# Kernel optimization log

Hardware: AMD Instinct MI355X
Metric: run time of the kernel (lower is better)

Reference implementation:

```python
import jax, jax.numpy as jnp
import numpy as np

F_CNT, V_CNT = 1024, 512
H, W = 192, 192
FX, FY = 200.0, 200.0
CX, CY = W / 2.0, H / 2.0
EPS = 1e-8


def quat_to_rot(q):
    # WXYZ quaternion -> rotation matrix, with normalization.
    q = q / (jnp.linalg.norm(q, axis=-1, keepdims=True) + EPS)
    w, x, y, z = q[..., 0], q[..., 1], q[..., 2], q[..., 3]
    return jnp.stack([
        jnp.stack([1 - 2 * (y * y + z * z), 2 * (x * y - w * z), 2 * (x * z + w * y)], -1),
        jnp.stack([2 * (x * y + w * z), 1 - 2 * (x * x + z * z), 2 * (y * z - w * x)], -1),
        jnp.stack([2 * (x * z - w * y), 2 * (y * z + w * x), 1 - 2 * (x * x + y * y)], -1),
    ], -2)


def rot_to_quat(R):
    # Branchless rotation matrix -> WXYZ quaternion.
    m00, m11, m22 = R[..., 0, 0], R[..., 1, 1], R[..., 2, 2]
    qw = 0.5 * jnp.sqrt(jnp.maximum(EPS, 1 + m00 + m11 + m22))
    qx = 0.5 * jnp.sqrt(jnp.maximum(EPS, 1 + m00 - m11 - m22))
    qy = 0.5 * jnp.sqrt(jnp.maximum(EPS, 1 - m00 + m11 - m22))
    qz = 0.5 * jnp.sqrt(jnp.maximum(EPS, 1 - m00 - m11 + m22))
    qx = jnp.copysign(qx, R[..., 2, 1] - R[..., 1, 2])
    qy = jnp.copysign(qy, R[..., 0, 2] - R[..., 2, 0])
    qz = jnp.copysign(qz, R[..., 1, 0] - R[..., 0, 1])
    return jnp.stack([qw, qx, qy, qz], -1)


def get_face_coord(a, b, c):
    # Per-face orthonormal frame (columns = x,y,z axes) and centroid.
    t = (a + b + c) / 3.0
    e1, e2 = b - a, c - a
    x = e1 / (jnp.linalg.norm(e1, axis=-1, keepdims=True) + EPS)
    n = jnp.cross(e1, e2)
    z = n / (jnp.linalg.norm(n, axis=-1, keepdims=True) + EPS)
    y = jnp.cross(z, x)
    return jnp.stack([x, y, z], -1), t


def render_gaussians(means, rot_qs, scales, colors, opac):
    # Differentiable 3DGS-style render: project, build 2D conics, depth-sorted
    # alpha compositing over all gaussians per pixel, white background.
    Rn = quat_to_rot(rot_qs)                      # [F,3,3]
    M = Rn * scales[:, None, :]                   # R @ diag(s)
    cov3 = M @ jnp.swapaxes(M, -1, -2)            # [F,3,3]
    X, Y, Z = means[:, 0], means[:, 1], means[:, 2]
    valid = (Z > 0.2).astype(means.dtype)
    Zc = jnp.maximum(Z, 0.2)
    mx = FX * X / Zc + CX
    my = FY * Y / Zc + CY
    zero = jnp.zeros_like(Zc)
    J = jnp.stack([
        jnp.stack([FX / Zc, zero, -FX * X / (Zc * Zc)], -1),
        jnp.stack([zero, FY / Zc, -FY * Y / (Zc * Zc)], -1),
    ], -2)                                        # [F,2,3]
    cov2 = J @ cov3 @ jnp.swapaxes(J, -1, -2)     # [F,2,2]
    a = cov2[:, 0, 0] + 0.3                       # low-pass dilation (3DGS)
    b = cov2[:, 0, 1]
    c = cov2[:, 1, 1] + 0.3
    det = jnp.maximum(a * c - b * b, EPS)
    conA, conB, conC = c / det, -b / det, a / det
    ys, xs = jnp.meshgrid(jnp.arange(H, dtype=means.dtype),
                          jnp.arange(W, dtype=means.dtype), indexing='ij')
    px, py = xs.reshape(-1), ys.reshape(-1)       # [HW]
    dx = px[None, :] - mx[:, None]                # [F,HW]
    dy = py[None, :] - my[:, None]
    power = -0.5 * (conA[:, None] * dx * dx + conC[:, None] * dy * dy) - conB[:, None] * dx * dy
    alpha = jnp.clip(opac[:, None] * jnp.exp(jnp.minimum(power, 0.0)), 0.0, 0.99) * valid[:, None]
    order = jnp.argsort(Zc)                       # front-to-back
    alpha = alpha[order]
    cols = colors[order]
    T = jnp.cumprod(1.0 - alpha, axis=0)
    T_excl = jnp.concatenate([jnp.ones_like(T[:1]), T[:-1]], axis=0)
    w = alpha * T_excl                            # [F,HW]
    img = jnp.einsum('fp,fc->cp', w, cols) + (1.0 - jnp.sum(w, 0))[None, :]
    return img.reshape(colors.shape[1], H, W)


def setup_inputs() -> dict:
    ks = jax.random.split(jax.random.key(0), 8)
    vp = jax.random.normal(ks[0], (V_CNT, 3), jnp.float32) * 0.5
    vp = vp.at[:, 2].add(5.0)  # put the mesh in front of the camera
    return {
        'img': jax.random.uniform(ks[1], (3, H, W), jnp.float32),
        'mask': jax.random.uniform(ks[2], (H, W), jnp.float32),
        'vertex_positions': vp,
        'faces': jax.random.randint(ks[3], (F_CNT, 3), 0, V_CNT, jnp.int32),
        'gp_rot_qs': jax.random.normal(ks[4], (F_CNT, 4), jnp.float32),
        'gp_log_scales': jax.random.normal(ks[5], (F_CNT, 3), jnp.float32) * 0.1 - 3.0,
        'gp_colors': jax.random.uniform(ks[6], (F_CNT, 3), jnp.float32),
        'gp_log_opacities': jnp.zeros((F_CNT, 1), jnp.float32),
    }


def reference(img, mask, vertex_positions, faces, gp_rot_qs, gp_log_scales,
              gp_colors, gp_log_opacities):
    vps_a = vertex_positions[faces[:, 0]]
    vps_b = vertex_positions[faces[:, 1]]
    vps_c = vertex_positions[faces[:, 2]]
    face_rs, face_ts = get_face_coord(vps_a, vps_b, vps_c)      # [F,3,3],[F,3]
    gp_scales = jnp.exp(gp_log_scales)
    gp_rot_mats = quat_to_rot(gp_rot_qs)
    # rows = scaled columns of the rotation (exactly as the torch code stacks)
    gp_rs = jnp.stack([gp_rot_mats[:, :, 0] * gp_scales[:, 0:1],
                       gp_rot_mats[:, :, 1] * gp_scales[:, 1:2],
                       gp_rot_mats[:, :, 2] * gp_scales[:, 2:3]], -2)
    global_gp_rs = face_rs @ gp_rs                               # merge_rt, gp_t = 0
    global_gp_ts = face_ts
    global_scales = jnp.linalg.norm(global_gp_rs, axis=-2)      # column norms [F,3]
    global_rot = global_gp_rs / (global_scales[:, None, :] + EPS)
    global_qs = rot_to_quat(global_rot)
    opac = jnp.exp(gp_log_opacities)[:, 0]
    rendered = render_gaussians(global_gp_ts, global_qs, global_scales, gp_colors, opac)
    mask_ = mask[None]
    masked_img = (1.0 - mask_) + img * mask_                     # white bg composite
    rgb_loss = jnp.mean((rendered - masked_img) ** 2)
    return rendered, rgb_loss
```

## Files before the change

kernel.cpp:

```cpp
#include <hip/hip_runtime.h>
#include <hip/hip_fp16.h>
#include <math.h>

#define F_CNT 1024
#define H_IMG 192
#define W_IMG 192
#define HW (H_IMG * W_IMG)
#define EPSF 1e-8f
#define N_SEG 8
#define SEG_LEN 128
#define HALF_PX 72
#define PIX_PER_BLK 144
#define LOG2E 1.4426950408889634f

#define RCP(x) __builtin_amdgcn_rcpf(x)


__device__ __forceinline__ unsigned long long prep_face(
    const int f,
    const float* __restrict__ vp,
    const int*   __restrict__ faces,
    const float* __restrict__ rot_qs,
    const float* __restrict__ log_scales,
    const float* __restrict__ colors,
    const float* __restrict__ log_opac,
    float sp[8][F_CNT])
{
    const int ia = faces[3 * f + 0], ib = faces[3 * f + 1], ic = faces[3 * f + 2];
    const float Ax = vp[3 * ia + 0], Ay = vp[3 * ia + 1], Az = vp[3 * ia + 2];
    const float Bx = vp[3 * ib + 0], By = vp[3 * ib + 1], Bz = vp[3 * ib + 2];
    const float Cx = vp[3 * ic + 0], Cy = vp[3 * ic + 1], Cz = vp[3 * ic + 2];

    const float tx = (Ax + Bx + Cx) / 3.0f;
    const float ty = (Ay + By + Cy) / 3.0f;
    const float tz = (Az + Bz + Cz) / 3.0f;

    const float e1x = Bx - Ax, e1y = By - Ay, e1z = Bz - Az;
    const float e2x = Cx - Ax, e2y = Cy - Ay, e2z = Cz - Az;

    const float rn1 = RCP(sqrtf(e1x * e1x + e1y * e1y + e1z * e1z) + EPSF);
    const float ux = e1x * rn1, uy = e1y * rn1, uz = e1z * rn1;
    const float cnx = e1y * e2z - e1z * e2y;
    const float cny = e1z * e2x - e1x * e2z;
    const float cnz = e1x * e2y - e1y * e2x;
    const float rn2 = RCP(sqrtf(cnx * cnx + cny * cny + cnz * cnz) + EPSF);
    const float wxv = cnx * rn2, wyv = cny * rn2, wzv = cnz * rn2;
    const float vx = wyv * uz - wzv * uy;
    const float vy = wzv * ux - wxv * uz;
    const float vz = wxv * uy - wyv * ux;

    const float q0 = rot_qs[4 * f + 0], q1 = rot_qs[4 * f + 1];
    const float q2 = rot_qs[4 * f + 2], q3 = rot_qs[4 * f + 3];
    const float rqn = RCP(sqrtf(q0 * q0 + q1 * q1 + q2 * q2 + q3 * q3) + EPSF);
    const float qw = q0 * rqn, qx = q1 * rqn, qy = q2 * rqn, qz = q3 * rqn;
    const float R00 = 1.0f - 2.0f * (qy * qy + qz * qz);
    const float R01 = 2.0f * (qx * qy - qw * qz);
    const float R02 = 2.0f * (qx * qz + qw * qy);
    const float R10 = 2.0f * (qx * qy + qw * qz);
    const float R11 = 1.0f - 2.0f * (qx * qx + qz * qz);
    const float R12 = 2.0f * (qy * qz - qw * qx);
    const float R20 = 2.0f * (qx * qz - qw * qy);
    const float R21 = 2.0f * (qy * qz + qw * qx);
    const float R22 = 1.0f - 2.0f * (qx * qx + qy * qy);

    const float s0 = expf(log_scales[3 * f + 0]);
    const float s1 = expf(log_scales[3 * f + 1]);
    const float s2 = expf(log_scales[3 * f + 2]);

    float G00, G10, G20, G01, G11, G21, G02, G12, G22;
    {
        float c0 = s0 * R00, c1 = s1 * R01, c2 = s2 * R02;
        G00 = ux * c0 + vx * c1 + wxv * c2;
        G10 = uy * c0 + vy * c1 + wyv * c2;
        G20 = uz * c0 + vz * c1 + wzv * c2;
    }
    {
        float c0 = s0 * R10, c1 = s1 * R11, c2 = s2 * R12;
        G01 = ux * c0 + vx * c1 + wxv * c2;
        G11 = uy * c0 + vy * c1 + wyv * c2;
        G21 = uz * c0 + vz * c1 + wzv * c2;
    }
    {
        float c0 = s0 * R20, c1 = s1 * R21, c2 = s2 * R22;
        G02 = ux * c0 + vx * c1 + wxv * c2;
        G12 = uy * c0 + vy * c1 + wyv * c2;
        G22 = uz * c0 + vz * c1 + wzv * c2;
    }

    const float gs0 = sqrtf(G00 * G00 + G10 * G10 + G20 * G20);
    const float gs1 = sqrtf(G01 * G01 + G11 * G11 + G21 * G21);
    const float gs2 = sqrtf(G02 * G02 + G12 * G12 + G22 * G22);
    const float rd0 = RCP(gs0 + EPSF), rd1 = RCP(gs1 + EPSF), rd2 = RCP(gs2 + EPSF);
    const float r00 = G00 * rd0, r10 = G10 * rd0, r20 = G20 * rd0;
    const float r01 = G01 * rd1, r11 = G11 * rd1, r21 = G21 * rd1;
    const float r02 = G02 * rd2, r12 = G12 * rd2, r22 = G22 * rd2;

    const float Qw = 0.5f * sqrtf(fmaxf(EPSF, 1.0f + r00 + r11 + r22));
    const float Qx = copysignf(0.5f * sqrtf(fmaxf(EPSF, 1.0f + r00 - r11 - r22)), r21 - r12);
    const float Qy = copysignf(0.5f * sqrtf(fmaxf(EPSF, 1.0f - r00 + r11 - r22)), r02 - r20);
    const float Qz = copysignf(0.5f * sqrtf(fmaxf(EPSF, 1.0f - r00 - r11 + r22)), r10 - r01);

    const float rqn2 = RCP(sqrtf(Qw * Qw + Qx * Qx + Qy * Qy + Qz * Qz) + EPSF);
    const float pw = Qw * rqn2, px = Qx * rqn2, py = Qy * rqn2, pz = Qz * rqn2;
    const float N00 = 1.0f - 2.0f * (py * py + pz * pz);
    const float N01 = 2.0f * (px * py - pw * pz);
    const float N02 = 2.0f * (px * pz + pw * py);
    const float N10 = 2.0f * (px * py + pw * pz);
    const float N11 = 1.0f - 2.0f * (px * px + pz * pz);
    const float N12 = 2.0f * (py * pz - pw * px);
    const float N20 = 2.0f * (px * pz - pw * py);
    const float N21 = 2.0f * (py * pz + pw * px);
    const float N22 = 1.0f - 2.0f * (px * px + py * py);

    const float M00 = N00 * gs0, M01 = N01 * gs1, M02 = N02 * gs2;
    const float M10 = N10 * gs0, M11 = N11 * gs1, M12 = N12 * gs2;
    const float M20 = N20 * gs0, M21 = N21 * gs1, M22 = N22 * gs2;
    const float C00 = M00 * M00 + M01 * M01 + M02 * M02;
    const float C01 = M00 * M10 + M01 * M11 + M02 * M12;
    const float C02 = M00 * M20 + M01 * M21 + M02 * M22;
    const float C11 = M10 * M10 + M11 * M11 + M12 * M12;
    const float C12 = M10 * M20 + M11 * M21 + M12 * M22;
    const float C22 = M20 * M20 + M21 * M21 + M22 * M22;

    const float valid = (tz > 0.2f) ? 1.0f : 0.0f;
    const float Zc = fmaxf(tz, 0.2f);
    const float rZc = RCP(Zc);
    const float mx = 200.0f * tx * rZc + 96.0f;
    const float my = 200.0f * ty * rZc + 96.0f;
    const float j00 = 200.0f * rZc;
    const float j02 = -200.0f * tx * (rZc * rZc);
    const float j11 = 200.0f * rZc;
    const float j12 = -200.0f * ty * (rZc * rZc);
    const float v00 = j00 * j00 * C00 + 2.0f * j00 * j02 * C02 + j02 * j02 * C22 + 0.3f;
    const float v01 = j00 * j11 * C01 + j00 * j12 * C02 + j02 * j11 * C12 + j02 * j12 * C22;
    const float v11 = j11 * j11 * C11 + 2.0f * j11 * j12 * C12 + j12 * j12 * C22 + 0.3f;
    const float rdet = RCP(fmaxf(v00 * v11 - v01 * v01, EPSF));
    const float conA = v11 * rdet, conB = -v01 * rdet, conC = v00 * rdet;
    const float opv = expf(log_opac[f]) * valid;

    const float LA = 0.5f * LOG2E * conA;
    const float LB = LOG2E * conB;
    const float LC = 0.5f * LOG2E * conC;
    const float t4 = fmaf(-LB, LB, 4.0f * LA * LC);
    const float reach2 = 140.0f * LA * RCP(fmaxf(t4, 1e-30f));

    union { __half2 h; float f; } c01u, cbo;
    c01u.h = __floats2half2_rn(colors[3 * f + 0], colors[3 * f + 1]);
    cbo.h  = __floats2half2_rn(colors[3 * f + 2], opv);

    sp[0][f] = mx;
    sp[1][f] = my;
    sp[2][f] = reach2;
    sp[3][f] = LA;
    sp[4][f] = LB;
    sp[5][f] = LC;
    sp[6][f] = c01u.f;
    sp[7][f] = cbo.f;

    return ((unsigned long long)__float_as_uint(Zc) << 32) | (unsigned int)f;
}

__device__ __forceinline__ void bstep(unsigned long long &kv, int j, int k, int tid)
{
    const unsigned long long pk = __shfl_xor(kv, j, 64);
    const bool keep_min = (((tid & k) == 0) == ((tid & j) == 0));
    kv = ((pk < kv) == keep_min) ? pk : kv;
}

__global__ __launch_bounds__(1024)
void fused_kernel(const float* __restrict__ vp,
                  const int*   __restrict__ faces,
                  const float* __restrict__ rot_qs,
                  const float* __restrict__ log_scales,
                  const float* __restrict__ colors,
                  const float* __restrict__ log_opac,
                  const float* __restrict__ img,
                  const float* __restrict__ mask,
                  float* __restrict__ out)
{
    __shared__ float  sp[8][F_CNT];
    __shared__ unsigned long long skv[F_CNT];
    __shared__ float4 lds4[F_CNT * 2];
    __shared__ unsigned int hlist[16][SEG_LEN];
    __shared__ float  lossb[PIX_PER_BLK];

    const int tid  = threadIdx.x;
    const int lane = tid & 63;
    const int wv   = tid >> 6;

    unsigned long long kv = prep_face(tid, vp, faces, rot_qs,
                                      log_scales, colors, log_opac, sp);

    #pragma unroll
    for (int k = 2; k <= 64; k <<= 1)
        #pragma unroll
        for (int j = k >> 1; j > 0; j >>= 1)
            bstep(kv, j, k, tid);

    skv[tid] = kv;
    __syncthreads();

    for (int k = 128; k <= F_CNT; k <<= 1) {
        for (int j = k >> 1; j >= 64; j >>= 1) {
            const int x = tid ^ j;
            if (x > tid) {
                const unsigned long long a  = skv[tid];
                const unsigned long long bb = skv[x];
                const bool up = ((tid & k) == 0);
                if (up ? (a > bb) : (a < bb)) { skv[tid] = bb; skv[x] = a; }
            }
            __syncthreads();
        }
        kv = skv[tid];
        #pragma unroll
        for (int j = 32; j > 0; j >>= 1)
            bstep(kv, j, k, tid);
        skv[tid] = kv;
        __syncthreads();
    }

    {
        const int src = (int)(skv[tid] & 0xffffffffULL);
        lds4[2 * tid + 0] = make_float4(sp[0][src], sp[1][src], sp[2][src], sp[3][src]);
        lds4[2 * tid + 1] = make_float4(sp[4][src], sp[5][src], sp[6][src], sp[7][src]);
        ((float2*)skv)[tid] = make_float2(sp[1][src], sp[2][src]);
    }
    __syncthreads();

    const int b   = blockIdx.x;
    const int pb1 = b * HALF_PX;
    const int pb2 = HW / 2 + b * HALF_PX;
    const int seg = wv & 7;
    const bool strip2 = (wv >= 8);
    const int pbase = strip2 ? pb2 : pb1;

    const float ra = (float)(pbase / W_IMG);
    const float rb = (float)((pbase + HALF_PX - 1) / W_IMG);

    int nhit;
    {
        const float4 tt = ((const float4*)skv)[seg * 64 + lane];

        const float dmA = fmaxf(0.0f, fmaxf(ra - tt.x, tt.x - rb));
        const float dmB = fmaxf(0.0f, fmaxf(ra - tt.z, tt.z - rb));
        const bool hA = dmA * dmA <= tt.y;
        const bool hB = dmB * dmB <= tt.w;

        const unsigned long long m0 = __ballot(hA);
        const unsigned long long m1 = __ballot(hB);
        const unsigned long long lt = (1ULL << lane) - 1ULL;
        const int pos0 = __popcll(m0 & lt) + __popcll(m1 & lt);
        const int pos1 = pos0 + (hA ? 1 : 0);
        if (hA) hlist[wv][pos0] = (unsigned)(2 * lane);
        if (hB) hlist[wv][pos1] = (unsigned)(2 * lane + 1);
        nhit = __popcll(m0) + __popcll(m1);
    }
    __syncthreads();

    const int p0 = pbase + lane, p1 = pbase + 64 + lane;
    const float fx0 = (float)(p0 % W_IMG), fy0 = (float)(p0 / W_IMG);
    const float fx1 = (float)(p1 % W_IMG), fy1 = (float)(p1 / W_IMG);

    float T0 = 1.0f, R0 = 0.0f, G0 = 0.0f, B0 = 0.0f;
    float T1 = 1.0f, R1 = 0.0f, G1 = 0.0f, B1 = 0.0f;

    const float4* __restrict__ Lb = lds4 + (seg << 8);
    for (int i = 0; i < nhit; ++i) {
        const int r = (int)hlist[wv][i];
        const float4 a  = Lb[2 * r + 0];
        const float4 bb = Lb[2 * r + 1];
        const float my = a.y;
        const float LA = a.w, LB = bb.x, LC = bb.y;
        union { float f; __half2 h; } urg, ubo;
        urg.f = bb.z;  ubo.f = bb.w;
        const float2 crg = __half22float2(urg.h);
        const float2 cbo = __half22float2(ubo.h);
        const float  cb  = cbo.x, opv = cbo.y;

        {
            const float dx = fx0 - a.x, dy = fy0 - my;
            const float t  = fmaf(LB, dy, LA * dx);
            const float u2 = (LC * dy) * dy;
            const float n  = -fmaf(t, dx, u2);
            const float e2 = exp2f(fminf(n, 0.0f));
            const float al = fminf(opv * e2, 0.99f);
            const float w  = al * T0;
            R0 = fmaf(w, crg.x, R0); G0 = fmaf(w, crg.y, G0); B0 = fmaf(w, cb, B0);
            T0 -= w;
        }
        {
            const float dx = fx1 - a.x, dy = fy1 - my;
            const float t  = fmaf(LB, dy, LA * dx);
            const float u2 = (LC * dy) * dy;
            const float n  = -fmaf(t, dx, u2);
            const float e2 = exp2f(fminf(n, 0.0f));
            const float al = fminf(opv * e2, 0.99f);
            const float w  = al * T1;
            R1 = fmaf(w, crg.x, R1); G1 = fmaf(w, crg.y, G1); B1 = fmaf(w, cb, B1);
            T1 -= w;
        }
    }

    __syncthreads();
    float4* __restrict__ fold4 = lds4;
    if (!strip2) {
        fold4[seg * PIX_PER_BLK + lane] = make_float4(R0, G0, B0, T0);
        if (lane < 8)
            fold4[seg * PIX_PER_BLK + 64 + lane] = make_float4(R1, G1, B1, T1);
    } else {
        fold4[seg * PIX_PER_BLK + 72 + lane] = make_float4(R0, G0, B0, T0);
        if (lane < 8)
            fold4[seg * PIX_PER_BLK + 136 + lane] = make_float4(R1, G1, B1, T1);
    }
    __syncthreads();

    float lsum = 0.0f;
    if (tid < PIX_PER_BLK) {
        float R = 0.0f, G = 0.0f, B = 0.0f, Tt = 1.0f;
        #pragma unroll
        for (int s = 0; s < N_SEG; ++s) {
            const float4 c = fold4[s * PIX_PER_BLK + tid];
            R += Tt * c.x; G += Tt * c.y; B += Tt * c.z;
            Tt *= c.w;
        }
        const float bg = Tt;
        const float o0 = R + bg, o1 = G + bg, o2 = B + bg;
        const int p = (tid < HALF_PX) ? (pb1 + tid) : (pb2 + tid - HALF_PX);
        out[p]          = o0;
        out[HW + p]     = o1;
        out[2 * HW + p] = o2;

        const float m = mask[p];
        const float base = 1.0f - m;
        const float e0 = o0 - (base + img[p] * m);
        const float e1 = o1 - (base + img[HW + p] * m);
        const float e2 = o2 - (base + img[2 * HW + p] * m);
        lsum = e0 * e0 + e1 * e1 + e2 * e2;
    }

    if (tid < PIX_PER_BLK) lossb[tid] = lsum;
    __syncthreads();
    if (tid < 64) {
        float s = lossb[tid] + lossb[tid + 64] + (tid < 16 ? lossb[tid + 128] : 0.0f);
        #pragma unroll
        for (int off = 32; off > 0; off >>= 1) s += __shfl_down(s, off);
        if (tid == 0)
            atomicAdd(out + 3 * HW, s * (1.0f / (float)(3 * HW)));
    }
}

extern "C" void kernel_launch(void* const* d_in, const int* in_sizes, int n_in,
                              void* d_out, int out_size, void* d_ws, size_t ws_size,
                              hipStream_t stream)
{
    const float* img        = (const float*)d_in[0];
    const float* mask       = (const float*)d_in[1];
    const float* vp         = (const float*)d_in[2];
    const int*   faces      = (const int*)d_in[3];
    const float* rot_qs     = (const float*)d_in[4];
    const float* log_scales = (const float*)d_in[5];
    const float* colors     = (const float*)d_in[6];
    const float* log_opac   = (const float*)d_in[7];
    float* out = (float*)d_out;

    hipMemsetAsync(out + 3 * HW, 0, sizeof(float), stream);

    fused_kernel<<<(HW / 2) / HALF_PX, 1024, 0, stream>>>(
        vp, faces, rot_qs, log_scales, colors, log_opac, img, mask, out);
}
```

Before: 101.0 us.

## Split fused kernel into prep-sort, partial render and combine kernels

Measured after the change: 100.9 us. No clear change (-0.1%).

```diff
diff --git a/kernel.cpp b/kernel.cpp
--- a/kernel.cpp
+++ b/kernel.cpp
@@ -16,16 +16,22 @@
 #define RCP(x) __builtin_amdgcn_rcpf(x)
 
 
-__device__ __forceinline__ unsigned long long prep_face(
-    const int f,
-    const float* __restrict__ vp,
-    const int*   __restrict__ faces,
-    const float* __restrict__ rot_qs,
-    const float* __restrict__ log_scales,
-    const float* __restrict__ colors,
-    const float* __restrict__ log_opac,
-    float sp[8][F_CNT])
+__global__ __launch_bounds__(1024)
+void prep_sort_kernel(const float* __restrict__ vp,
+                      const int*   __restrict__ faces,
+                      const float* __restrict__ rot_qs,
+                      const float* __restrict__ log_scales,
+                      const float* __restrict__ colors,
+                      const float* __restrict__ log_opac,
+                      float* __restrict__ params,
+                      float* __restrict__ out)
 {
+    __shared__ float sp[8][F_CNT];
+    __shared__ unsigned long long skv[F_CNT];
+
+    const int f = threadIdx.x;
+    if (f == 0) out[3 * HW] = 0.0f;
+
     const int ia = faces[3 * f + 0], ib = faces[3 * f + 1], ic = faces[3 * f + 2];
     const float Ax = vp[3 * ia + 0], Ay = vp[3 * ia + 1], Az = vp[3 * ia + 2];
     const float Bx = vp[3 * ib + 0], By = vp[3 * ib + 1], Bz = vp[3 * ib + 2];
@@ -157,90 +163,87 @@
     sp[6][f] = c01u.f;
     sp[7][f] = cbo.f;
 
-    return ((unsigned long long)__float_as_uint(Zc) << 32) | (unsigned int)f;
+    unsigned long long kv =
+        ((unsigned long long)__float_as_uint(Zc) << 32) | (unsigned int)f;
+
+    #pragma unroll
+    for (int k = 2; k <= 64; k <<= 1)
+        #pragma unroll
+        for (int j = k >> 1; j > 0; j >>= 1) {
+            const unsigned long long pk = __shfl_xor(kv, j, 64);
+            const bool keep_min = (((f & k) == 0) == ((f & j) == 0));
+            kv = ((pk < kv) == keep_min) ? pk : kv;
+        }
+
+    skv[f] = kv;
+    __syncthreads();
+
+    for (int k = 128; k <= F_CNT; k <<= 1) {
+        for (int j = k >> 1; j >= 64; j >>= 1) {
+            const int x = f ^ j;
+            if (x > f) {
+                const unsigned long long a  = skv[f];
+                const unsigned long long bb = skv[x];
+                const bool up = ((f & k) == 0);
+                if (up ? (a > bb) : (a < bb)) { skv[f] = bb; skv[x] = a; }
+            }
+            __syncthreads();
+        }
+        kv = skv[f];
+        #pragma unroll
+        for (int j = 32; j > 0; j >>= 1) {
+            const unsigned long long pk = __shfl_xor(kv, j, 64);
+            const bool keep_min = (((f & k) == 0) == ((f & j) == 0));
+            kv = ((pk < kv) == keep_min) ? pk : kv;
+        }
+        skv[f] = kv;
+        __syncthreads();
+    }
+
+    const int src = (int)(skv[f] & 0xffffffffULL);
+    float4* __restrict__ d4 = (float4*)params + 2 * f;
+    d4[0] = make_float4(sp[0][src], sp[1][src], sp[2][src], sp[3][src]);
+    d4[1] = make_float4(sp[4][src], sp[5][src], sp[6][src], sp[7][src]);
 }
 
-__device__ __forceinline__ void bstep(unsigned long long &kv, int j, int k, int tid)
+__global__ __launch_bounds__(512)
+void render_partial_kernel(const float* __restrict__ params,
+                           float* __restrict__ partials)
 {
-    const unsigned long long pk = __shfl_xor(kv, j, 64);
-    const bool keep_min = (((tid & k) == 0) == ((tid & j) == 0));
-    kv = ((pk < kv) == keep_min) ? pk : kv;
-}
-
-__global__ __launch_bounds__(1024)
-void fused_kernel(const float* __restrict__ vp,
-                  const int*   __restrict__ faces,
-                  const float* __restrict__ rot_qs,
-                  const float* __restrict__ log_scales,
-                  const float* __restrict__ colors,
-                  const float* __restrict__ log_opac,
-                  const float* __restrict__ img,
-                  const float* __restrict__ mask,
-                  float* __restrict__ out)
-{
-    __shared__ float  sp[8][F_CNT];
-    __shared__ unsigned long long skv[F_CNT];
-    __shared__ float4 lds4[F_CNT * 2];
-    __shared__ unsigned int hlist[16][SEG_LEN];
-    __shared__ float  lossb[PIX_PER_BLK];
+    __shared__ float4 lds4[1024];
+    __shared__ float2 myr[512];
+    __shared__ unsigned int hlist[8][SEG_LEN];
 
     const int tid  = threadIdx.x;
     const int lane = tid & 63;
     const int wv   = tid >> 6;
 
-    unsigned long long kv = prep_face(tid, vp, faces, rot_qs,
-                                      log_scales, colors, log_opac, sp);
-
-    #pragma unroll
-    for (int k = 2; k <= 64; k <<= 1)
-        #pragma unroll
-        for (int j = k >> 1; j > 0; j >>= 1)
-            bstep(kv, j, k, tid);
-
-    skv[tid] = kv;
+    const int bid = blockIdx.x;
+    const int h   = bid >> 8;
+    const int r   = (bid + (h ? 128 : 0)) & 255;
+
+    {
+        const float4* __restrict__ rec4 = (const float4*)params;
+        const float4 a  = rec4[2 * (512 * h + tid) + 0];
+        const float4 bb = rec4[2 * (512 * h + tid) + 1];
+        lds4[2 * tid + 0] = a;
+        lds4[2 * tid + 1] = bb;
+        myr[tid] = make_float2(a.y, a.z);
+    }
     __syncthreads();
 
-    for (int k = 128; k <= F_CNT; k <<= 1) {
-        for (int j = k >> 1; j >= 64; j >>= 1) {
-            const int x = tid ^ j;
-            if (x > tid) {
-                const unsigned long long a  = skv[tid];
-                const unsigned long long bb = skv[x];
-                const bool up = ((tid & k) == 0);
-                if (up ? (a > bb) : (a < bb)) { skv[tid] = bb; skv[x] = a; }
-            }
-            __syncthreads();
-        }
-        kv = skv[tid];
-        #pragma unroll
-        for (int j = 32; j > 0; j >>= 1)
-            bstep(kv, j, k, tid);
-        skv[tid] = kv;
-        __syncthreads();
-    }
-
-    {
-        const int src = (int)(skv[tid] & 0xffffffffULL);
-        lds4[2 * tid + 0] = make_float4(sp[0][src], sp[1][src], sp[2][src], sp[3][src]);
-        lds4[2 * tid + 1] = make_float4(sp[4][src], sp[5][src], sp[6][src], sp[7][src]);
-        ((float2*)skv)[tid] = make_float2(sp[1][src], sp[2][src]);
-    }
-    __syncthreads();
-
-    const int b   = blockIdx.x;
-    const int pb1 = b * HALF_PX;
-    const int pb2 = HW / 2 + b * HALF_PX;
-    const int seg = wv & 7;
-    const bool strip2 = (wv >= 8);
-    const int pbase = strip2 ? pb2 : pb1;
+    const int pb1 = r * HALF_PX;
+    const int pb2 = HW / 2 + r * HALF_PX;
+    const int seg_l  = wv & 3;
+    const bool strip2 = (wv >= 4);
+    const int pbase  = strip2 ? pb2 : pb1;
 
     const float ra = (float)(pbase / W_IMG);
     const float rb = (float)((pbase + HALF_PX - 1) / W_IMG);
 
     int nhit;
     {
-        const float4 tt = ((const float4*)skv)[seg * 64 + lane];
-
+        const float4 tt = ((const float4*)myr)[seg_l * 64 + lane];
         const float dmA = fmaxf(0.0f, fmaxf(ra - tt.x, tt.x - rb));
         const float dmB = fmaxf(0.0f, fmaxf(ra - tt.z, tt.z - rb));
         const bool hA = dmA * dmA <= tt.y;
@@ -264,11 +267,11 @@
     float T0 = 1.0f, R0 = 0.0f, G0 = 0.0f, B0 = 0.0f;
     float T1 = 1.0f, R1 = 0.0f, G1 = 0.0f, B1 = 0.0f;
 
-    const float4* __restrict__ Lb = lds4 + (seg << 8);
+    const float4* __restrict__ Lb = lds4 + (seg_l << 8);
     for (int i = 0; i < nhit; ++i) {
-        const int r = (int)hlist[wv][i];
-        const float4 a  = Lb[2 * r + 0];
-        const float4 bb = Lb[2 * r + 1];
+        const int rr = (int)hlist[wv][i];
+        const float4 a  = Lb[2 * rr + 0];
+        const float4 bb = Lb[2 * rr + 1];
         const float my = a.y;
         const float LA = a.w, LB = bb.x, LC = bb.y;
         union { float f; __half2 h; } urg, ubo;
@@ -301,27 +304,36 @@
         }
     }
 
-    __syncthreads();
-    float4* __restrict__ fold4 = lds4;
-    if (!strip2) {
-        fold4[seg * PIX_PER_BLK + lane] = make_float4(R0, G0, B0, T0);
-        if (lane < 8)
-            fold4[seg * PIX_PER_BLK + 64 + lane] = make_float4(R1, G1, B1, T1);
-    } else {
-        fold4[seg * PIX_PER_BLK + 72 + lane] = make_float4(R0, G0, B0, T0);
-        if (lane < 8)
-            fold4[seg * PIX_PER_BLK + 136 + lane] = make_float4(R1, G1, B1, T1);
-    }
-    __syncthreads();
+    float4* __restrict__ part = (float4*)partials;
+    const int gseg = 4 * h + seg_l;
+    const int base = (r * N_SEG + gseg) * PIX_PER_BLK + (strip2 ? HALF_PX : 0);
+    part[base + lane] = make_float4(R0, G0, B0, T0);
+    if (lane < 8)
+        part[base + 64 + lane] = make_float4(R1, G1, B1, T1);
+}
+
+__global__ __launch_bounds__(256)
+void combine_kernel(const float* __restrict__ partials,
+                    const float* __restrict__ img,
+                    const float* __restrict__ mask,
+                    float* __restrict__ out)
+{
+    __shared__ float lossb[PIX_PER_BLK];
+
+    const int tid = threadIdx.x;
+    const int c   = blockIdx.x;
+    const int pb1 = c * HALF_PX;
+    const int pb2 = HW / 2 + c * HALF_PX;
 
     float lsum = 0.0f;
     if (tid < PIX_PER_BLK) {
+        const float4* __restrict__ part = (const float4*)partials;
         float R = 0.0f, G = 0.0f, B = 0.0f, Tt = 1.0f;
         #pragma unroll
         for (int s = 0; s < N_SEG; ++s) {
-            const float4 c = fold4[s * PIX_PER_BLK + tid];
-            R += Tt * c.x; G += Tt * c.y; B += Tt * c.z;
-            Tt *= c.w;
+            const float4 cc = part[(c * N_SEG + s) * PIX_PER_BLK + tid];
+            R += Tt * cc.x; G += Tt * cc.y; B += Tt * cc.z;
+            Tt *= cc.w;
         }
         const float bg = Tt;
         const float o0 = R + bg, o1 = G + bg, o2 = B + bg;
@@ -361,10 +373,12 @@
     const float* log_scales = (const float*)d_in[5];
     const float* colors     = (const float*)d_in[6];
     const float* log_opac   = (const float*)d_in[7];
-    float* out = (float*)d_out;
-
-    hipMemsetAsync(out + 3 * HW, 0, sizeof(float), stream);
-
-    fused_kernel<<<(HW / 2) / HALF_PX, 1024, 0, stream>>>(
-        vp, faces, rot_qs, log_scales, colors, log_opac, img, mask, out);
+    float* out      = (float*)d_out;
+    float* params   = (float*)d_ws;
+    float* partials = (float*)d_ws + 8192;
+
+    prep_sort_kernel<<<1, F_CNT, 0, stream>>>(vp, faces, rot_qs, log_scales,
+                                              colors, log_opac, params, out);
+    render_partial_kernel<<<512, 512, 0, stream>>>(params, partials);
+    combine_kernel<<<256, 256, 0, stream>>>(partials, img, mask, out);
 }
```
